# Performance work log

Hardware: AMD Instinct MI355X
Metric: run time of the kernel (lower is better)

The kernel has to match this reference:

```python
import jax, jax.numpy as jnp
import numpy as np

NHRZ, BATCH, NU, NY, NH = 2048, 128, 64, 64, 256  # NH even; half-size rotation params


def setup_inputs() -> dict:
    key = jax.random.key(0)
    ks = jax.random.split(key, 9)
    H = NH // 2
    damping = 0.9  # dampingConstantInitial < 1.0
    return {
        "y0": jax.random.normal(ks[0], (BATCH, NY), jnp.float32),
        "U": jax.random.normal(ks[1], (NHRZ, BATCH, NU), jnp.float32),
        # torch init: lmbd_cont_real = -log(damping) * ones(H); imag ~ U[0,1)
        "lmbd_cont_real": jnp.full((H,), -np.log(damping), jnp.float32),
        "lmbd_cont_imag": jax.random.uniform(ks[2], (H,), jnp.float32),
        "B": jax.random.normal(ks[3], (NH, NU), jnp.float32) / np.sqrt(NU),
        "Wy2x": jax.random.normal(ks[4], (NH, NY), jnp.float32) / np.sqrt(NY),
        "by2x": jax.random.normal(ks[5], (NH,), jnp.float32) * 0.01,
        "Wx2y": jax.random.normal(ks[6], (NY, NH), jnp.float32) / np.sqrt(NH),
        "bx2y": jax.random.normal(ks[7], (NY,), jnp.float32) * 0.01,
    }


def reference(y0, U, lmbd_cont_real, lmbd_cont_imag, B, Wy2x, by2x, Wx2y, bx2y):
    H = lmbd_cont_real.shape[0]  # Nhidden // 2
    r = jnp.exp(-jnp.abs(lmbd_cont_real))
    theta = (np.pi / 2) * lmbd_cont_imag
    lr = r * jnp.cos(theta)   # [H]
    li = r * jnp.sin(theta)   # [H]
    nf = jnp.sqrt(1.0 - jnp.exp(-2.0 * jnp.abs(lmbd_cont_real)))
    nf2 = jnp.concatenate((nf, nf))                       # [2H]
    Bu = jnp.einsum('tbu,hu->tbh', U, B) * nf2            # [T, B, 2H]
    x0 = y0 @ Wy2x.T + by2x                               # [B, 2H]

    # A = [[diag(lr), -diag(li)], [diag(li), diag(lr)]]; x_new = x @ A.T = A x
    def step(x, bu):
        x1, x2 = x[..., :H], x[..., H:]
        xn = jnp.concatenate((lr * x1 - li * x2, li * x1 + lr * x2), axis=-1) + bu
        return xn, xn

    _, Xs = jax.lax.scan(step, x0, Bu)                    # [T, B, 2H]
    X = jnp.concatenate((x0[None], Xs), axis=0)           # [T+1, B, 2H]
    Y = X @ Wx2y.T + bx2y                                 # [T+1, B, Ny]
    return Y
```

## Files before the change

kernel.cpp:

```cpp
#include <hip/hip_runtime.h>
#include <hip/hip_bf16.h>

typedef __bf16 bf16x8 __attribute__((ext_vector_type(8)));
typedef __bf16 bf16x4 __attribute__((ext_vector_type(4)));
typedef float  f32x4  __attribute__((ext_vector_type(4)));

constexpr int kNHRZ = 2048, kBATCH = 128, kNU = 64, kNY = 64, kNH = 256, kH = 128;
constexpr int kCHUNK = 256, kNCHUNK = kNHRZ / kCHUNK;
constexpr int kTS = 16, kBT = 2, kM = kTS * kBT;
constexpr int kNSUB = kCHUNK / kTS;

constexpr int U_STR  = 72;
constexpr int BT_STR = 36;
constexpr int X_STR  = 264;

constexpr int OFF_U  = 0;
constexpr int OFF_BU = OFF_U + kM * U_STR * 2;
constexpr int OFF_X  = OFF_BU + kNH * BT_STR * 2;
constexpr int SMEM1  = OFF_X;
constexpr int SMEM2  = OFF_X + kM * X_STR * 2;

__device__ inline bf16x8 pack8(float4 a, float4 b) {
    bf16x8 v;
    v[0] = (__bf16)a.x; v[1] = (__bf16)a.y; v[2] = (__bf16)a.z; v[3] = (__bf16)a.w;
    v[4] = (__bf16)b.x; v[5] = (__bf16)b.y; v[6] = (__bf16)b.z; v[7] = (__bf16)b.w;
    return v;
}

template <bool FINAL>
__global__ __launch_bounds__(256, 2) void scan_mfma(
    const float* __restrict__ U,
    const float* __restrict__ lre,
    const float* __restrict__ lim,
    const float* __restrict__ Bmat,
    const float* __restrict__ Wx2y,
    const float* __restrict__ bx2y,
    const float* __restrict__ starts,
    float* __restrict__ ends,
    float* __restrict__ out)
{
    extern __shared__ char smem[];
    __bf16* Us  = (__bf16*)(smem + OFF_U);
    __bf16* BuT = (__bf16*)(smem + OFF_BU);
    __bf16* Xs  = (__bf16*)(smem + OFF_X);

    const int tid  = threadIdx.x;
    const int lane = tid & 63;
    const int w    = tid >> 6;
    const int lw   = lane & 15;
    const int lg   = lane >> 4;
    const int blk  = blockIdx.x;
    const int c    = blk >> 6;
    const int bp   = blk & 63;
    const int bglob = bp * 2;
    const int t0   = c * kCHUNK;

    bf16x8 Bf[2][4];
#pragma unroll
    for (int nt = 0; nt < 4; ++nt) {
        const int h  = w * 64 + nt * 16 + lw;
        const float ab = fabsf(lre[h & (kH - 1)]);
        const float nf = sqrtf(fmaxf(0.0f, 1.0f - expf(-2.0f * ab)));
#pragma unroll
        for (int ks = 0; ks < 2; ++ks) {
            const float* p = Bmat + h * kNU + ks * 32 + lg * 8;
            float4 f0 = ((const float4*)p)[0];
            float4 f1 = ((const float4*)p)[1];
            f0.x *= nf; f0.y *= nf; f0.z *= nf; f0.w *= nf;
            f1.x *= nf; f1.y *= nf; f1.z *= nf; f1.w *= nf;
            Bf[ks][nt] = pack8(f0, f1);
        }
    }

    bf16x8 Wf[8][2];
    float  bias[2] = {0.f, 0.f};
    if constexpr (FINAL) {
#pragma unroll
        for (int nt = 0; nt < 2; ++nt) {
            const int y = (w >> 1) * 32 + nt * 16 + lw;
            bias[nt] = bx2y[y];
#pragma unroll
            for (int ks = 0; ks < 8; ++ks) {
                const float* p = Wx2y + y * kNH + ks * 32 + lg * 8;
                Wf[ks][nt] = pack8(((const float4*)p)[0], ((const float4*)p)[1]);
            }
        }
    }

    const int hm = tid & 127;
    const int bl = tid >> 7;
    float lr, li;
    {
        const float ab = fabsf(lre[hm]);
        const float r  = expf(-ab);
        const float th = 1.5707963267948966f * lim[hm];
        lr = r * cosf(th);
        li = r * sinf(th);
    }
    float x1, x2;
    if constexpr (FINAL) {
        const size_t sb = ((size_t)c * kBATCH + bglob + bl) * kNH;
        x1 = starts[sb + hm];
        x2 = starts[sb + hm + kH];
    } else {
        x1 = 0.0f; x2 = 0.0f;
    }

    const int sm = tid >> 3, sq = tid & 7;
    const int st_t = sm & 15, st_b = sm >> 4;
    const float* uptr0 =
        U + ((size_t)(t0 + st_t) * kBATCH + (bglob + st_b)) * kNU + sq * 8;

    float4 u0 = ((const float4*)uptr0)[0];
    float4 u1 = ((const float4*)uptr0)[1];

#pragma unroll 1
    for (int s = 0; s < kNSUB; ++s) {
        *(bf16x8*)&Us[sm * U_STR + sq * 8] = pack8(u0, u1);
        if (s + 1 < kNSUB) {
            const float* p = uptr0 + (size_t)(s + 1) * kTS * kBATCH * kNU;
            u0 = ((const float4*)p)[0];
            u1 = ((const float4*)p)[1];
        }
        __syncthreads();

        {
            f32x4 acc[2][4] = {};
#pragma unroll
            for (int ks = 0; ks < 2; ++ks) {
                bf16x8 a0 = *(const bf16x8*)&Us[(lw)      * U_STR + ks * 32 + lg * 8];
                bf16x8 a1 = *(const bf16x8*)&Us[(16 + lw) * U_STR + ks * 32 + lg * 8];
#pragma unroll
                for (int nt = 0; nt < 4; ++nt) {
                    acc[0][nt] = __builtin_amdgcn_mfma_f32_16x16x32_bf16(a0, Bf[ks][nt], acc[0][nt], 0, 0, 0);
                    acc[1][nt] = __builtin_amdgcn_mfma_f32_16x16x32_bf16(a1, Bf[ks][nt], acc[1][nt], 0, 0, 0);
                }
            }
#pragma unroll
            for (int mt = 0; mt < 2; ++mt)
#pragma unroll
                for (int nt = 0; nt < 4; ++nt) {
                    bf16x4 v;
                    v[0] = (__bf16)acc[mt][nt][0]; v[1] = (__bf16)acc[mt][nt][1];
                    v[2] = (__bf16)acc[mt][nt][2]; v[3] = (__bf16)acc[mt][nt][3];
                    *(bf16x4*)&BuT[(w * 64 + nt * 16 + lw) * BT_STR + mt * 16 + lg * 4] = v;
                }
        }
        __syncthreads();

        {
            bf16x4 qr[4], qi[4];
#pragma unroll
            for (int k = 0; k < 4; ++k) {
                qr[k] = *(const bf16x4*)&BuT[hm * BT_STR + bl * 16 + k * 4];
                qi[k] = *(const bf16x4*)&BuT[(hm + kH) * BT_STR + bl * 16 + k * 4];
            }
#pragma unroll
            for (int t = 0; t < kTS; ++t) {
                const float bu1 = (float)qr[t >> 2][t & 3];
                const float bu2 = (float)qi[t >> 2][t & 3];
                const float n1 = fmaf(lr, x1, fmaf(-li, x2, bu1));
                const float n2 = fmaf(li, x1, fmaf(lr, x2, bu2));
                x1 = n1; x2 = n2;
                if constexpr (FINAL) {
                    const int m = bl * 16 + t;
                    Xs[m * X_STR + hm]      = (__bf16)x1;
                    Xs[m * X_STR + kH + hm] = (__bf16)x2;
                }
            }
        }

        if constexpr (FINAL) {
            __syncthreads();
            f32x4 acc2[2] = {};
            const int mtY = w & 1;
#pragma unroll
            for (int ks = 0; ks < 8; ++ks) {
                bf16x8 a = *(const bf16x8*)&Xs[(mtY * 16 + lw) * X_STR + ks * 32 + lg * 8];
                acc2[0] = __builtin_amdgcn_mfma_f32_16x16x32_bf16(a, Wf[ks][0], acc2[0], 0, 0, 0);
                acc2[1] = __builtin_amdgcn_mfma_f32_16x16x32_bf16(a, Wf[ks][1], acc2[1], 0, 0, 0);
            }
#pragma unroll
            for (int i = 0; i < 4; ++i) {
                const int t = t0 + s * kTS + lg * 4 + i;
                float* orow = out + ((size_t)(1 + t) * kBATCH + bglob + mtY) * kNY +
                              (w >> 1) * 32 + lw;
#pragma unroll
                for (int nt = 0; nt < 2; ++nt)
                    orow[nt * 16] = acc2[nt][i] + bias[nt];
            }
        }
    }

    if constexpr (!FINAL) {
        const size_t eb = ((size_t)c * kBATCH + bglob + bl) * kNH;
        ends[eb + hm]      = x1;
        ends[eb + hm + kH] = x2;
    }
}

__global__ __launch_bounds__(128) void combine_kernel(
    const float* __restrict__ y0, const float* __restrict__ Wy2x,
    const float* __restrict__ by2x, const float* __restrict__ lre,
    const float* __restrict__ lim, const float* __restrict__ ends,
    float* __restrict__ starts)
{
    const int b  = blockIdx.x;
    const int hm = threadIdx.x;

    const float ab = fabsf(lre[hm]);
    const float r  = expf(-ab);
    const float th = 1.5707963267948966f * lim[hm];
    float lr = r * cosf(th);
    float li = r * sinf(th);
    float pr = lr, pi = li;
#pragma unroll
    for (int k = 0; k < 8; ++k) {
        const float nr = pr * pr - pi * pi;
        const float ni = 2.0f * pr * pi;
        pr = nr; pi = ni;
    }

    float s1 = by2x[hm];
    float s2 = by2x[hm + kH];
#pragma unroll 8
    for (int q = 0; q < kNY; ++q) {
        const float yv = y0[b * kNY + q];
        s1 = fmaf(Wy2x[hm * kNY + q], yv, s1);
        s2 = fmaf(Wy2x[(hm + kH) * kNY + q], yv, s2);
    }

    for (int c = 0; c < kNCHUNK; ++c) {
        const size_t base = ((size_t)c * kBATCH + b) * kNH;
        starts[base + hm]      = s1;
        starts[base + hm + kH] = s2;
        const float e1 = ends[base + hm];
        const float e2 = ends[base + hm + kH];
        const float n1 = fmaf(pr, s1, fmaf(-pi, s2, e1));
        const float n2 = fmaf(pi, s1, fmaf(pr, s2, e2));
        s1 = n1; s2 = n2;
    }
}

__global__ __launch_bounds__(64) void y0_kernel(
    const float* __restrict__ starts, const float* __restrict__ Wx2y,
    const float* __restrict__ bx2y, float* __restrict__ out)
{
    const int b = blockIdx.x;
    const int y = threadIdx.x;
    const float* x0 = starts + (size_t)b * kNH;
    float acc = bx2y[y];
#pragma unroll 4
    for (int h = 0; h < kNH; h += 4) {
        float4 xv = *(const float4*)&x0[h];
        float4 wv = *(const float4*)&Wx2y[y * kNH + h];
        acc = fmaf(wv.x, xv.x, acc);
        acc = fmaf(wv.y, xv.y, acc);
        acc = fmaf(wv.z, xv.z, acc);
        acc = fmaf(wv.w, xv.w, acc);
    }
    out[(size_t)b * kNY + y] = acc;
}

extern "C" void kernel_launch(void* const* d_in, const int* in_sizes, int n_in,
                              void* d_out, int out_size, void* d_ws, size_t ws_size,
                              hipStream_t stream) {
    const float* y0   = (const float*)d_in[0];
    const float* U    = (const float*)d_in[1];
    const float* lre  = (const float*)d_in[2];
    const float* lim  = (const float*)d_in[3];
    const float* Bmat = (const float*)d_in[4];
    const float* Wy2x = (const float*)d_in[5];
    const float* by2x = (const float*)d_in[6];
    const float* Wx2y = (const float*)d_in[7];
    const float* bx2y = (const float*)d_in[8];
    float* out = (float*)d_out;

    float* ends   = (float*)d_ws;
    float* starts = ends + (size_t)kNCHUNK * kBATCH * kNH;

    const int grid = kNCHUNK * (kBATCH / kBT);

    scan_mfma<false><<<grid, 256, SMEM1, stream>>>(
        U, lre, lim, Bmat, nullptr, nullptr, nullptr, ends, nullptr);
    combine_kernel<<<kBATCH, 128, 0, stream>>>(
        y0, Wy2x, by2x, lre, lim, ends, starts);
    y0_kernel<<<kBATCH, 64, 0, stream>>>(starts, Wx2y, bx2y, out);
    scan_mfma<true><<<grid, 256, SMEM2, stream>>>(
        U, lre, lim, Bmat, Wx2y, bx2y, starts, nullptr, out);
}
```

Measured before the change: 76.89 us.

## Remap waves so each owns its Bu slice, double-buffer U, drop barrier

Each wave now computes the Bu projection for one batch row and a 64-wide slice of both real and imaginary hidden halves. These are exactly the values it later scans, so the barrier between the MFMA write of BuT and the scan read is removed. The U staging buffer is double-buffered to stay safe without that barrier, and the next U global load is issued later (after the MFMAs or after the output barrier) so it overlaps other work. The cost is more B fragments held in registers per wave (16 bf16x8 instead of 8), which may hurt occupancy under the 2-blocks-per-CU launch bound.

```diff
diff --git a/kernel.cpp b/kernel.cpp
--- a/kernel.cpp
+++ b/kernel.cpp
@@ -15,7 +15,7 @@
 constexpr int X_STR  = 264;
 
 constexpr int OFF_U  = 0;
-constexpr int OFF_BU = OFF_U + kM * U_STR * 2;
+constexpr int OFF_BU = OFF_U + 2 * kM * U_STR * 2;
 constexpr int OFF_X  = OFF_BU + kNH * BT_STR * 2;
 constexpr int SMEM1  = OFF_X;
 constexpr int SMEM2  = OFF_X + kM * X_STR * 2;
@@ -49,17 +49,20 @@
     const int w    = tid >> 6;
     const int lw   = lane & 15;
     const int lg   = lane >> 4;
+    const int bl   = w >> 1;
+    const int hh   = w & 1;
     const int blk  = blockIdx.x;
     const int c    = blk >> 6;
     const int bp   = blk & 63;
     const int bglob = bp * 2;
     const int t0   = c * kCHUNK;
 
-    bf16x8 Bf[2][4];
-#pragma unroll
-    for (int nt = 0; nt < 4; ++nt) {
-        const int h  = w * 64 + nt * 16 + lw;
-        const float ab = fabsf(lre[h & (kH - 1)]);
+    bf16x8 Bf[2][8];
+#pragma unroll
+    for (int nt = 0; nt < 8; ++nt) {
+        const int hre = hh * 64 + (nt & 3) * 16 + lw;
+        const int h   = hre + (nt >> 2) * kH;
+        const float ab = fabsf(lre[hre]);
         const float nf = sqrtf(fmaxf(0.0f, 1.0f - expf(-2.0f * ab)));
 #pragma unroll
         for (int ks = 0; ks < 2; ++ks) {
@@ -87,8 +90,7 @@
         }
     }
 
-    const int hm = tid & 127;
-    const int bl = tid >> 7;
+    const int hm = hh * 64 + lane;
     float lr, li;
     {
         const float ab = fabsf(lre[hm]);
@@ -116,37 +118,39 @@
 
 #pragma unroll 1
     for (int s = 0; s < kNSUB; ++s) {
-        *(bf16x8*)&Us[sm * U_STR + sq * 8] = pack8(u0, u1);
-        if (s + 1 < kNSUB) {
-            const float* p = uptr0 + (size_t)(s + 1) * kTS * kBATCH * kNU;
-            u0 = ((const float4*)p)[0];
-            u1 = ((const float4*)p)[1];
-        }
+        __bf16* Uc = Us + (s & 1) * (kM * U_STR);
+
+        *(bf16x8*)&Uc[sm * U_STR + sq * 8] = pack8(u0, u1);
         __syncthreads();
 
         {
-            f32x4 acc[2][4] = {};
-#pragma unroll
-            for (int ks = 0; ks < 2; ++ks) {
-                bf16x8 a0 = *(const bf16x8*)&Us[(lw)      * U_STR + ks * 32 + lg * 8];
-                bf16x8 a1 = *(const bf16x8*)&Us[(16 + lw) * U_STR + ks * 32 + lg * 8];
-#pragma unroll
-                for (int nt = 0; nt < 4; ++nt) {
-                    acc[0][nt] = __builtin_amdgcn_mfma_f32_16x16x32_bf16(a0, Bf[ks][nt], acc[0][nt], 0, 0, 0);
-                    acc[1][nt] = __builtin_amdgcn_mfma_f32_16x16x32_bf16(a1, Bf[ks][nt], acc[1][nt], 0, 0, 0);
+            bf16x8 A0 = *(const bf16x8*)&Uc[(bl * 16 + lw) * U_STR + 0 * 32 + lg * 8];
+            bf16x8 A1 = *(const bf16x8*)&Uc[(bl * 16 + lw) * U_STR + 1 * 32 + lg * 8];
+            f32x4 acc[8] = {};
+#pragma unroll
+            for (int nt = 0; nt < 8; ++nt)
+                acc[nt] = __builtin_amdgcn_mfma_f32_16x16x32_bf16(A0, Bf[0][nt], acc[nt], 0, 0, 0);
+#pragma unroll
+            for (int nt = 0; nt < 8; ++nt)
+                acc[nt] = __builtin_amdgcn_mfma_f32_16x16x32_bf16(A1, Bf[1][nt], acc[nt], 0, 0, 0);
+
+            if constexpr (!FINAL) {
+                if (s + 1 < kNSUB) {
+                    const float* p = uptr0 + (size_t)(s + 1) * kTS * kBATCH * kNU;
+                    u0 = ((const float4*)p)[0];
+                    u1 = ((const float4*)p)[1];
                 }
             }
-#pragma unroll
-            for (int mt = 0; mt < 2; ++mt)
-#pragma unroll
-                for (int nt = 0; nt < 4; ++nt) {
-                    bf16x4 v;
-                    v[0] = (__bf16)acc[mt][nt][0]; v[1] = (__bf16)acc[mt][nt][1];
-                    v[2] = (__bf16)acc[mt][nt][2]; v[3] = (__bf16)acc[mt][nt][3];
-                    *(bf16x4*)&BuT[(w * 64 + nt * 16 + lw) * BT_STR + mt * 16 + lg * 4] = v;
-                }
-        }
-        __syncthreads();
+
+#pragma unroll
+            for (int nt = 0; nt < 8; ++nt) {
+                const int h = hh * 64 + (nt & 3) * 16 + lw + (nt >> 2) * kH;
+                bf16x4 v;
+                v[0] = (__bf16)acc[nt][0]; v[1] = (__bf16)acc[nt][1];
+                v[2] = (__bf16)acc[nt][2]; v[3] = (__bf16)acc[nt][3];
+                *(bf16x4*)&BuT[h * BT_STR + bl * 16 + lg * 4] = v;
+            }
+        }
 
         {
             bf16x4 qr[4], qi[4];
@@ -172,6 +176,11 @@
 
         if constexpr (FINAL) {
             __syncthreads();
+            if (s + 1 < kNSUB) {
+                const float* p = uptr0 + (size_t)(s + 1) * kTS * kBATCH * kNU;
+                u0 = ((const float4*)p)[0];
+                u1 = ((const float4*)p)[1];
+            }
             f32x4 acc2[2] = {};
             const int mtY = w & 1;
 #pragma unroll
```

Measured after the change: 86.40 us. 12.4% more time.
